# Kernel tuning notes

Measured on AMD Instinct MI355X. Metric: run time of the kernel, lower is better.

Reference implementation:

```python
import jax, jax.numpy as jnp
import numpy as np

N, B, H, L, FE = 32768, 256, 128, 4, 4
E = 262144


def setup_inputs() -> dict:
    key = jax.random.key(0)
    ks = jax.random.split(key, 16)
    def g(i, shape, scale=0.05):
        return jax.random.normal(ks[i], shape, dtype=jnp.float32) * scale
    return {
        "d": jax.random.uniform(ks[0], (E,), dtype=jnp.float32) * 5.0,
        "src": jax.random.randint(ks[1], (E,), 0, N),
        "dst": jax.random.randint(ks[2], (E,), 0, N),
        "seg": jnp.sort(jax.random.randint(ks[3], (N,), 0, B)),
        "node_emb": g(4, (H,), 1.0),
        "We": g(5, (2 * FE + 1, H)), "be": jnp.zeros((H,), jnp.float32),
        "msg_W1": g(6, (L, 3 * H, H)), "msg_b1": jnp.zeros((L, H), jnp.float32),
        "msg_W2": g(7, (L, H, H)), "msg_b2": jnp.zeros((L, H), jnp.float32),
        "soft_W": g(8, (L, H)), "soft_b": jnp.zeros((L,), jnp.float32),
        "upd_W1": g(9, (L, H, H)), "upd_b1": jnp.zeros((L, H), jnp.float32),
        "upd_W2": g(10, (L, H, H)), "upd_b2": jnp.zeros((L, H), jnp.float32),
        "out_W1": g(11, (H, H)), "out_b1": jnp.zeros((H,), jnp.float32),
        "out_W2": g(12, (H, H)), "out_b2": jnp.zeros((H,), jnp.float32),
    }


def reference(d, src, dst, seg, node_emb, We, be, msg_W1, msg_b1, msg_W2, msg_b2,
              soft_W, soft_b, upd_W1, upd_b1, upd_W2, upd_b2,
              out_W1, out_b1, out_W2, out_b2):
    silu = jax.nn.silu
    # fourier_encode_dist: [E] -> [E, 2*FE+1] = [sin(d/2^k), cos(d/2^k), d]
    scales = 2.0 ** jnp.arange(FE, dtype=d.dtype)
    x = d[:, None] / scales
    de = jnp.concatenate([jnp.sin(x), jnp.cos(x), d[:, None]], axis=-1)
    # edge_input MLP (1 layer, last_activation=SiLU) then extra F.silu in input_edge_func
    e = silu(silu(de @ We + be))                              # [E, H]
    # node_embedding broadcast to all nodes
    feat = jnp.broadcast_to(node_emb, (N, H))
    for l in range(L):
        mi = jnp.concatenate([feat[src], feat[dst], e], axis=-1)        # [E, 3H]
        m = silu(silu(mi @ msg_W1[l] + msg_b1[l]) @ msg_W2[l] + msg_b2[l])  # [E, H]
        e = e + m                                             # edge residual update
        w = jax.nn.sigmoid(m @ soft_W[l] + soft_b[l])[:, None]  # soft edge gate [E,1]
        msum = jax.ops.segment_sum(m * w, dst, num_segments=N)  # reduce to dst nodes
        upd_in = msum + feat
        feat = silu(upd_in @ upd_W1[l] + upd_b1[l]) @ upd_W2[l] + upd_b2[l] + feat
    # node-wise output network (2 layers, last activation None)
    feat = silu(feat @ out_W1 + out_b1) @ out_W2 + out_b2
    # multi-aggregator readout over graphs in batch
    s = jax.ops.segment_sum(feat, seg, num_segments=B)
    cnt = jax.ops.segment_sum(jnp.ones((N, 1), feat.dtype), seg, num_segments=B)
    mean = s / jnp.maximum(cnt, 1.0)
    mx = jax.ops.segment_max(feat, seg, num_segments=B)
    return jnp.concatenate([s, mean, mx], axis=-1)            # [B, 3H]
```

## Files before the change

kernel.cpp:

```cpp
#include <hip/hip_runtime.h>
#include <hip/hip_bf16.h>

#define NN 32768
#define NB 256
#define HD 128
#define NL 4
#define NE 262144

typedef short bf16x8 __attribute__((ext_vector_type(8)));
typedef float f32x4 __attribute__((ext_vector_type(4)));
typedef unsigned short u16;
typedef unsigned int u32;

__device__ __forceinline__ float bf2f(u16 u) {
  return __uint_as_float(((u32)u) << 16);
}
__device__ __forceinline__ u16 f2bf(float f) {
  u32 x = __float_as_uint(f);
  u32 r = x + 0x7FFFu + ((x >> 16) & 1u);
  return (u16)(r >> 16);
}
__device__ __forceinline__ u32 pk2(float a, float b) {
  __hip_bfloat162 h = __float22bfloat162_rn(make_float2(a, b));
  return *reinterpret_cast<u32*>(&h);
}
__device__ __forceinline__ float siluf(float x) {
  return x * __builtin_amdgcn_rcpf(1.0f + __expf(-x));
}
__device__ __forceinline__ float sigf(float x) {
  return __builtin_amdgcn_rcpf(1.0f + __expf(-x));
}
__device__ __forceinline__ u32 ordu(float f) {
  u32 b = __float_as_uint(f);
  return (b & 0x80000000u) ? ~b : (b | 0x80000000u);
}

__device__ __forceinline__ float ldinf(const void* p, size_t i, int mode) {
  return mode ? ((const float*)p)[i] : bf2f(((const u16*)p)[i]);
}
__device__ __forceinline__ u16 ldinb(const void* p, size_t i, int mode) {
  return mode ? f2bf(((const float*)p)[i]) : ((const u16*)p)[i];
}

__global__ void k_detect(const u16* __restrict__ Weraw, int* __restrict__ flag) {
  if (threadIdx.x == 0 && blockIdx.x == 0) {
    int cnt = 0;
    for (int i = 0; i < 256; i++) {
      u16 u = Weraw[2 * i];
      u32 e = (u >> 7) & 0xFFu;
      if (e >= 112u && e <= 126u) cnt++;
    }
    *flag = (cnt >= 128) ? 0 : 1;
  }
}


__global__ __launch_bounds__(256) void k_csr_deg(const int* __restrict__ dstp,
                                                 u32* __restrict__ deg) {
  const int i = blockIdx.x * 256 + threadIdx.x;
  atomicAdd(&deg[dstp[i]], 1u);
}

__global__ __launch_bounds__(1024) void k_csr_scan(const u32* __restrict__ deg,
                                                   int* __restrict__ rowptr,
                                                   int* __restrict__ cursor) {
  __shared__ int part[1024];
  const int t = threadIdx.x;
  int loc[32];
  int s = 0;
#pragma unroll
  for (int j = 0; j < 32; j++) { loc[j] = s; s += (int)deg[t * 32 + j]; }
  part[t] = s;
  __syncthreads();
  int inc = s;
  for (int off = 1; off < 1024; off <<= 1) {
    int tmp = (t >= off) ? part[t - off] : 0;
    __syncthreads();
    part[t] += tmp;
    __syncthreads();
  }
  const int base = part[t] - inc;
#pragma unroll
  for (int j = 0; j < 32; j++) {
    rowptr[t * 32 + j] = base + loc[j];
    cursor[t * 32 + j] = base + loc[j];
  }
  if (t == 1023) rowptr[NN] = part[1023];
}

__global__ __launch_bounds__(256) void k_csr_scatter(const int* __restrict__ dstp,
                                                     const int* __restrict__ srcp,
                                                     int* __restrict__ cursor,
                                                     int* __restrict__ eids,
                                                     int* __restrict__ src_s,
                                                     int* __restrict__ dst_s) {
  const int i = blockIdx.x * 256 + threadIdx.x;
  const int d = dstp[i];
  const int pos = atomicAdd(&cursor[d], 1);
  eids[pos] = i;
  src_s[pos] = srcp[i];
  dst_s[pos] = d;
}

#define PANEL 16384

template <int MT>
__device__ __forceinline__ void acc_zero(f32x4 (&acc)[MT][8]) {
#pragma unroll
  for (int mt = 0; mt < MT; mt++)
#pragma unroll
    for (int nt = 0; nt < 8; nt++) acc[mt][nt] = f32x4{0.f, 0.f, 0.f, 0.f};
}

template <int MT>
__device__ __forceinline__ void gemm_gp(const u16* __restrict__ A0,
                                        const size_t* rowoff,
                                        const u16* __restrict__ Bp,
                                        int l, int kg, f32x4 (&acc)[MT][8]) {
#pragma unroll
  for (int ks = 0; ks < 4; ks++) {
    bf16x8 a[MT];
#pragma unroll
    for (int mt = 0; mt < MT; mt++)
      a[mt] = *(const bf16x8*)&A0[rowoff[mt] + ks * 32 + kg * 8];
#pragma unroll
    for (int nt = 0; nt < 8; nt++) {
      bf16x8 b = *(const bf16x8*)&Bp[(size_t)((nt * 4 + ks) * 64 + l) * 8];
#pragma unroll
      for (int mt = 0; mt < MT; mt++)
        acc[mt][nt] = __builtin_amdgcn_mfma_f32_16x16x32_bf16(a[mt], b, acc[mt][nt], 0, 0, 0);
    }
  }
}

template <int MT>
__device__ __forceinline__ void wave_gemm_p(const short* lAw, const u16* __restrict__ Bp,
                                            int l, int c, int kg, f32x4 (&acc)[MT][8]) {
#pragma unroll
  for (int ks = 0; ks < 4; ks++) {
    bf16x8 a[MT];
#pragma unroll
    for (int mt = 0; mt < MT; mt++) {
      const int r = mt * 16 + c;
      const int k = ks * 32 + kg * 8;
      a[mt] = *(const bf16x8*)&lAw[r * HD + (k ^ ((r & 7) << 3))];
    }
#pragma unroll
    for (int nt = 0; nt < 8; nt++) {
      bf16x8 b = *(const bf16x8*)&Bp[(size_t)((nt * 4 + ks) * 64 + l) * 8];
#pragma unroll
      for (int mt = 0; mt < MT; mt++)
        acc[mt][nt] = __builtin_amdgcn_mfma_f32_16x16x32_bf16(a[mt], b, acc[mt][nt], 0, 0, 0);
    }
  }
}

template <int MT, bool SILU>
__device__ __forceinline__ void wave_pack(short* lAw, int c, int kg,
                                          f32x4 (&acc)[MT][8], const float* bias) {
#pragma unroll
  for (int mt = 0; mt < MT; mt++) {
#pragma unroll
    for (int rr = 0; rr < 4; rr++) {
      const int row = mt * 16 + kg * 4 + rr;
      u32 ou[4];
#pragma unroll
      for (int p = 0; p < 4; p++) {
        float x0 = acc[mt][2 * p][rr] + bias[2 * p];
        float x1 = acc[mt][2 * p + 1][rr] + bias[2 * p + 1];
        if (SILU) { x0 = siluf(x0); x1 = siluf(x1); }
        ou[p] = pk2(x0, x1);
      }
      ((int4*)(lAw + row * HD))[c ^ (row & 7)] =
          make_int4((int)ou[0], (int)ou[1], (int)ou[2], (int)ou[3]);
    }
  }
}

__global__ __launch_bounds__(256) void k_prep(
    const void* __restrict__ mW1, const void* __restrict__ mW2,
    const void* __restrict__ uW1, const void* __restrict__ uW2,
    const void* __restrict__ oW1, const void* __restrict__ oW2,
    const int* __restrict__ flagp,
    u16* __restrict__ Wt1, u16* __restrict__ Wt2p,
    u16* __restrict__ Wtu1, u16* __restrict__ Wtu2p,
    u16* __restrict__ Wto1, u16* __restrict__ Wto2p) {
  const int mode = *flagp;
  const int tid = blockIdx.x * blockDim.x + threadIdx.x;
  const int stride = gridDim.x * blockDim.x;
  for (int i = tid; i < NL * 3 * PANEL; i += stride) {
    const int l = i / (3 * PANEL), r = i % (3 * PANEL);
    const int chunk = r / PANEL, r2 = r % PANEL;
    const int nt = r2 / 2048, ks = (r2 % 2048) / 512;
    const int lane = (r2 % 512) / 8, j = r2 % 8;
    const int s = ks * 32 + (lane >> 4) * 8 + j;
    const int klog = ((s & 7) << 4) | (s >> 3);
    const int n = nt * 16 + (lane & 15);
    Wt1[i] = ldinb(mW1, ((size_t)l * 384 + chunk * 128 + klog) * HD + n, mode);
  }
  for (int i = tid; i < NL * PANEL; i += stride) {
    const int l = i / PANEL, r = i % PANEL;
    const int nt = r / 2048, ks = (r % 2048) / 512;
    const int lane = (r % 512) / 8, j = r % 8;
    const int s = ks * 32 + (lane >> 4) * 8 + j;
    const int klog = ((s & 7) << 4) | (s >> 3);
    const int n = nt * 16 + (lane & 15);
    Wt2p[i] = ldinb(mW2, ((size_t)l * HD + klog) * HD + n, mode);
    Wtu1[i] = ldinb(uW1, ((size_t)l * HD + klog) * HD + n, mode);
    Wtu2p[i] = ldinb(uW2, ((size_t)l * HD + klog) * HD + n, mode);
  }
  for (int i = tid; i < PANEL; i += stride) {
    const int nt = i / 2048, ks = (i % 2048) / 512;
    const int lane = (i % 512) / 8, j = i % 8;
    const int s = ks * 32 + (lane >> 4) * 8 + j;
    const int klog = ((s & 7) << 4) | (s >> 3);
    const int n = nt * 16 + (lane & 15);
    Wto1[i] = ldinb(oW1, (size_t)klog * HD + n, mode);
    Wto2p[i] = ldinb(oW2, (size_t)klog * HD + n, mode);
  }
}

__global__ __launch_bounds__(256) void k_featinit(const void* __restrict__ nemb,
                                                  const int* __restrict__ flagp,
                                                  u16* __restrict__ feat) {
  const int mode = *flagp;
  const int i = blockIdx.x * 256 + threadIdx.x;
  const int g = i & 15;
  u32 ou[4];
#pragma unroll
  for (int p = 0; p < 4; p++) {
    u16 a = ldinb(nemb, (2 * p) * 16 + g, mode);
    u16 b = ldinb(nemb, (2 * p + 1) * 16 + g, mode);
    ou[p] = (u32)a | ((u32)b << 16);
  }
  ((int4*)feat)[i] = make_int4((int)ou[0], (int)ou[1], (int)ou[2], (int)ou[3]);
}

__global__ __launch_bounds__(256) void k_encode(const void* __restrict__ d,
                                                const int* __restrict__ eids,
                                                const void* __restrict__ We,
                                                const void* __restrict__ be,
                                                const int* __restrict__ flagp,
                                                u16* __restrict__ e) {
  const int mode = *flagp;
  __shared__ float sW[9 * HD];
  __shared__ float sb[HD];
  for (int i = threadIdx.x; i < 9 * HD; i += 256) sW[i] = ldinf(We, i, mode);
  for (int i = threadIdx.x; i < HD; i += 256) sb[i] = ldinf(be, i, mode);
  __syncthreads();
  const int spos = blockIdx.x * 256 + threadIdx.x;
  const float dv = ldinf(d, eids[spos], mode);
  float de[9];
#pragma unroll
  for (int k = 0; k < 4; k++) {
    float x = dv * (1.0f / (float)(1 << k));
    de[k] = __sinf(x);
    de[4 + k] = __cosf(x);
  }
  de[8] = dv;
  u16* erow = e + (size_t)spos * HD;
#pragma unroll
  for (int g = 0; g < 16; g++) {
    u32 ou[4];
#pragma unroll
    for (int p = 0; p < 4; p++) {
      float vv[2];
#pragma unroll
      for (int t = 0; t < 2; t++) {
        const int h = (2 * p + t) * 16 + g;
        float a = sb[h];
#pragma unroll
        for (int k = 0; k < 9; k++) a += de[k] * sW[k * HD + h];
        vv[t] = siluf(siluf(a));
      }
      ou[p] = pk2(vv[0], vv[1]);
    }
    ((int4*)erow)[g] = make_int4((int)ou[0], (int)ou[1], (int)ou[2], (int)ou[3]);
  }
}

__global__ __launch_bounds__(64, 4) void k_edge(
    const u16* __restrict__ feat, u16* __restrict__ e,
    const int* __restrict__ src_s, const int* __restrict__ dst_s,
    const u16* __restrict__ Wt1, const u16* __restrict__ Wt2p,
    const void* __restrict__ b1g, const void* __restrict__ b2g,
    const void* __restrict__ softW, const void* __restrict__ softb,
    const int* __restrict__ flagp, float* __restrict__ msum, int layer) {
  __shared__ __align__(16) short lM[32 * HD];
  __shared__ float swg[32];
  __shared__ int sdst[32];
  const int mode = *flagp;
  const int l = threadIdx.x;
  const int c = l & 15, kg = l >> 4;
  const int blk = blockIdx.x * 32;

  if (l < 32) sdst[l] = dst_s[blk + l];

  size_t offS[2], offD[2], offE[2];
#pragma unroll
  for (int mt = 0; mt < 2; mt++) {
    const int eidx = blk + mt * 16 + c;
    offS[mt] = (size_t)src_s[eidx] * HD;
    offD[mt] = (size_t)dst_s[eidx] * HD;
    offE[mt] = (size_t)eidx * HD;
  }

  const u16* W1l = Wt1 + (size_t)layer * 3 * PANEL;
  const u16* W2l = Wt2p + (size_t)layer * PANEL;
  float bias1[8], bias2[8], swf[8];
#pragma unroll
  for (int nt = 0; nt < 8; nt++) {
    bias1[nt] = ldinf(b1g, layer * HD + nt * 16 + c, mode);
    bias2[nt] = ldinf(b2g, layer * HD + nt * 16 + c, mode);
    swf[nt] = ldinf(softW, (size_t)layer * HD + nt * 16 + c, mode);
  }
  const float sbv = ldinf(softb, layer, mode);

  f32x4 acc[2][8];
  acc_zero<2>(acc);
  gemm_gp<2>(feat, offS, W1l, l, kg, acc);
  gemm_gp<2>(feat, offD, W1l + PANEL, l, kg, acc);
  gemm_gp<2>(e, offE, W1l + 2 * PANEL, l, kg, acc);
  wave_pack<2, true>(lM, c, kg, acc, bias1);
  __syncthreads();

  acc_zero<2>(acc);
  wave_gemm_p<2>(lM, W2l, l, c, kg, acc);
  __syncthreads();

  float wred[2][4];
#pragma unroll
  for (int mt = 0; mt < 2; mt++) {
#pragma unroll
    for (int rr = 0; rr < 4; rr++) {
      const int row = mt * 16 + kg * 4 + rr;
      int4* erow4 = (int4*)(e + (size_t)(blk + row) * HD);
      const int4 eo = erow4[c];
      const u32 eu[4] = {(u32)eo.x, (u32)eo.y, (u32)eo.z, (u32)eo.w};
      float mv[8];
      float wp = 0.f;
#pragma unroll
      for (int nt = 0; nt < 8; nt++) {
        mv[nt] = siluf(acc[mt][nt][rr] + bias2[nt]);
        wp += mv[nt] * swf[nt];
      }
      u32 mo[4], ou[4];
#pragma unroll
      for (int p = 0; p < 4; p++) {
        mo[p] = pk2(mv[2 * p], mv[2 * p + 1]);
        ou[p] = pk2(bf2f((u16)(eu[p] & 0xffffu)) + mv[2 * p],
                    bf2f((u16)(eu[p] >> 16)) + mv[2 * p + 1]);
      }
      ((int4*)(lM + row * HD))[c ^ (row & 7)] =
          make_int4((int)mo[0], (int)mo[1], (int)mo[2], (int)mo[3]);
      erow4[c] = make_int4((int)ou[0], (int)ou[1], (int)ou[2], (int)ou[3]);
      wp += __shfl_xor(wp, 1);
      wp += __shfl_xor(wp, 2);
      wp += __shfl_xor(wp, 4);
      wp += __shfl_xor(wp, 8);
      wred[mt][rr] = wp;
    }
  }
#pragma unroll
  for (int mt = 0; mt < 2; mt++)
#pragma unroll
    for (int rr = 0; rr < 4; rr++)
      if (c == mt * 4 + rr) swg[mt * 16 + kg * 4 + rr] = sigf(wred[mt][rr] + sbv);
  __syncthreads();

  const int gM = ((l >> 3) << 3);
  const int em = l & 7;
  float a0 = 0.f, a1 = 0.f;
  int cur = sdst[0];
  for (int r = 0; r < 32; r++) {
    const int dn = sdst[r];
    if (dn != cur) {
      atomicAdd(&msum[(size_t)cur * HD + l], a0);
      atomicAdd(&msum[(size_t)cur * HD + l + 64], a1);
      a0 = 0.f; a1 = 0.f; cur = dn;
    }
    const int rx = (r & 7) << 3;
    const float wgr = swg[r];
    a0 += wgr * bf2f((u16)lM[r * HD + (gM ^ rx) + em]);
    a1 += wgr * bf2f((u16)lM[r * HD + (gM ^ rx) + 64 + em]);
  }
  atomicAdd(&msum[(size_t)cur * HD + l], a0);
  atomicAdd(&msum[(size_t)cur * HD + l + 64], a1);
}

__global__ __launch_bounds__(64, 4) void k_node(
    u16* __restrict__ feat, const float* __restrict__ msum,
    const u16* __restrict__ Wtu1, const u16* __restrict__ Wtu2p,
    const void* __restrict__ b1g, const void* __restrict__ b2g,
    const int* __restrict__ flagp, int layer) {
  __shared__ __align__(16) short lA[32 * HD];
  const int mode = *flagp;
  const int l = threadIdx.x;
  const int c = l & 15, kg = l >> 4;
  short* lAw = lA;
  const int blkn = blockIdx.x * 32;
  const u16* W1l = Wtu1 + (size_t)layer * PANEL;
  const u16* W2l = Wtu2p + (size_t)layer * PANEL;
  float bias1[8], bias2[8];
#pragma unroll
  for (int nt = 0; nt < 8; nt++) {
    bias1[nt] = ldinf(b1g, layer * HD + nt * 16 + c, mode);
    bias2[nt] = ldinf(b2g, layer * HD + nt * 16 + c, mode);
  }
#pragma unroll
  for (int rp = 0; rp < 8; rp++) {
    const int r = rp * 4 + (l >> 4);
    const int g = l & 15;
    const int4 fv = ((const int4*)(feat + (size_t)(blkn + r) * HD))[g];
    const u32 uu[4] = {(u32)fv.x, (u32)fv.y, (u32)fv.z, (u32)fv.w};
    const float4 ma = ((const float4*)(msum + (size_t)(blkn + r) * HD))[2 * g];
    const float4 mb = ((const float4*)(msum + (size_t)(blkn + r) * HD))[2 * g + 1];
    const float mm[8] = {ma.x, ma.y, ma.z, ma.w, mb.x, mb.y, mb.z, mb.w};
    u32 ou[4];
#pragma unroll
    for (int p = 0; p < 4; p++) {
      ou[p] = pk2(bf2f((u16)(uu[p] & 0xffffu)) + mm[2 * p],
                  bf2f((u16)(uu[p] >> 16)) + mm[2 * p + 1]);
    }
    ((int4*)(lAw + r * HD))[g ^ (r & 7)] =
        make_int4((int)ou[0], (int)ou[1], (int)ou[2], (int)ou[3]);
  }
  __syncthreads();
  f32x4 acc[2][8];
  acc_zero<2>(acc);
  wave_gemm_p<2>(lAw, W1l, l, c, kg, acc);
  __syncthreads();
  wave_pack<2, true>(lAw, c, kg, acc, bias1);
  __syncthreads();
  acc_zero<2>(acc);
  wave_gemm_p<2>(lAw, W2l, l, c, kg, acc);

#pragma unroll
  for (int mt = 0; mt < 2; mt++) {
#pragma unroll
    for (int rr = 0; rr < 4; rr++) {
      const int row = mt * 16 + kg * 4 + rr;
      int4* frow4 = (int4*)(feat + (size_t)(blkn + row) * HD);
      const int4 fo = frow4[c];
      const u32 fu[4] = {(u32)fo.x, (u32)fo.y, (u32)fo.z, (u32)fo.w};
      u32 ou[4];
#pragma unroll
      for (int p = 0; p < 4; p++) {
        const float x0 = acc[mt][2 * p][rr] + bias2[2 * p];
        const float x1 = acc[mt][2 * p + 1][rr] + bias2[2 * p + 1];
        ou[p] = pk2(bf2f((u16)(fu[p] & 0xffffu)) + x0,
                    bf2f((u16)(fu[p] >> 16)) + x1);
      }
      frow4[c] = make_int4((int)ou[0], (int)ou[1], (int)ou[2], (int)ou[3]);
    }
  }
}

__global__ __launch_bounds__(64, 4) void k_out(
    const u16* __restrict__ feat, const int* __restrict__ seg,
    const u16* __restrict__ Wto1, const u16* __restrict__ Wto2p,
    const void* __restrict__ ob1, const void* __restrict__ ob2,
    const int* __restrict__ flagp,
    float* __restrict__ sacc, u32* __restrict__ mxacc, float* __restrict__ cnt) {
  __shared__ __align__(16) short lA[32 * HD];
  __shared__ int sseg[32];
  const int mode = *flagp;
  const int l = threadIdx.x;
  const int c = l & 15, kg = l >> 4;
  short* lAw = lA;
  const int blkn = blockIdx.x * 32;
  float bias1[8], bias2[8];
#pragma unroll
  for (int nt = 0; nt < 8; nt++) {
    bias1[nt] = ldinf(ob1, nt * 16 + c, mode);
    bias2[nt] = ldinf(ob2, nt * 16 + c, mode);
  }
#pragma unroll
  for (int rp = 0; rp < 8; rp++) {
    const int r = rp * 4 + (l >> 4);
    const int g = l & 15;
    ((int4*)(lAw + r * HD))[g ^ (r & 7)] =
        ((const int4*)(feat + (size_t)(blkn + r) * HD))[g];
  }
  if (l < 32) sseg[l] = seg[blkn + l];
  __syncthreads();
  f32x4 acc[2][8];
  acc_zero<2>(acc);
  wave_gemm_p<2>(lAw, Wto1, l, c, kg, acc);
  __syncthreads();
  wave_pack<2, true>(lAw, c, kg, acc, bias1);
  __syncthreads();
  acc_zero<2>(acc);
  wave_gemm_p<2>(lAw, Wto2p, l, c, kg, acc);
  __syncthreads();
  wave_pack<2, false>(lAw, c, kg, acc, bias2);
  __syncthreads();

  const int gL = l >> 2;
  const int eoff = (l & 3) * 2;
  const bool uniform = (sseg[0] == sseg[31]);
  if (uniform) {
    const int g = sseg[0];
    float s1 = 0.f, s2 = 0.f, x1 = -3.402823e38f, x2 = -3.402823e38f;
#pragma unroll 4
    for (int r = 0; r < 32; r++) {
      const u32 mv = *(const u32*)&lAw[r * HD + ((gL ^ (r & 7)) << 3) + eoff];
      const float v1 = bf2f((u16)(mv & 0xffffu));
      const float v2 = bf2f((u16)(mv >> 16));
      s1 += v1; s2 += v2;
      x1 = fmaxf(x1, v1); x2 = fmaxf(x2, v2);
    }
    atomicAdd(&sacc[(size_t)g * HD + 2 * l], s1);
    atomicAdd(&sacc[(size_t)g * HD + 2 * l + 1], s2);
    atomicMax(&mxacc[(size_t)g * HD + 2 * l], ordu(x1));
    atomicMax(&mxacc[(size_t)g * HD + 2 * l + 1], ordu(x2));
    if (l == 0) atomicAdd(&cnt[g], 32.0f);
  } else {
    if (l < 32) atomicAdd(&cnt[sseg[l]], 1.0f);
#pragma unroll 4
    for (int r = 0; r < 32; r++) {
      const u32 mv = *(const u32*)&lAw[r * HD + ((gL ^ (r & 7)) << 3) + eoff];
      const float v1 = bf2f((u16)(mv & 0xffffu));
      const float v2 = bf2f((u16)(mv >> 16));
      const int g = sseg[r];
      atomicAdd(&sacc[(size_t)g * HD + 2 * l], v1);
      atomicAdd(&sacc[(size_t)g * HD + 2 * l + 1], v2);
      atomicMax(&mxacc[(size_t)g * HD + 2 * l], ordu(v1));
      atomicMax(&mxacc[(size_t)g * HD + 2 * l + 1], ordu(v2));
    }
  }
}

__global__ __launch_bounds__(256) void k_final(const float* __restrict__ sacc,
                                               const u32* __restrict__ mxacc,
                                               const float* __restrict__ cnt,
                                               const int* __restrict__ flagp,
                                               void* __restrict__ out) {
  const int mode = *flagp;
  const int i = blockIdx.x * 256 + threadIdx.x;
  const int b = i / 384, j = i % 384;
  float v;
  if (j < HD) {
    const int p = ((j & 15) << 3) | (j >> 4);
    v = sacc[b * HD + p];
  } else if (j < 2 * HD) {
    const int t = j - HD;
    const int p = ((t & 15) << 3) | (t >> 4);
    v = sacc[b * HD + p] / fmaxf(cnt[b], 1.0f);
  } else {
    const int t = j - 2 * HD;
    const int p = ((t & 15) << 3) | (t >> 4);
    u32 u = mxacc[b * HD + p];
    u32 bits = (u >> 31) ? (u ^ 0x80000000u) : ~u;
    v = __uint_as_float(bits);
  }
  if (mode) ((float*)out)[i] = v;
  else ((u16*)out)[i] = f2bf(v);
}

extern "C" void kernel_launch(void* const* d_in, const int* in_sizes, int n_in,
                              void* d_out, int out_size, void* d_ws, size_t ws_size,
                              hipStream_t stream) {
  const void* d_d = d_in[0];
  const int* src = (const int*)d_in[1];
  const int* dst = (const int*)d_in[2];
  const int* seg = (const int*)d_in[3];
  const void* nemb = d_in[4];
  const void* We = d_in[5];
  const void* be = d_in[6];
  const void* mW1 = d_in[7];
  const void* mb1 = d_in[8];
  const void* mW2 = d_in[9];
  const void* mb2 = d_in[10];
  const void* sW = d_in[11];
  const void* sb = d_in[12];
  const void* uW1 = d_in[13];
  const void* ub1 = d_in[14];
  const void* uW2 = d_in[15];
  const void* ub2 = d_in[16];
  const void* oW1 = d_in[17];
  const void* ob1 = d_in[18];
  const void* oW2 = d_in[19];
  const void* ob2 = d_in[20];

  char* ws = (char*)d_ws;
  const size_t OFF_E = 0;
  const size_t OFF_MSUM = OFF_E + (size_t)NE * HD * 2;
  const size_t OFF_FEAT = OFF_MSUM + (size_t)NN * HD * 4;
  const size_t OFF_SACC = OFF_FEAT + (size_t)NN * HD * 2;
  const size_t OFF_MX = OFF_SACC + (size_t)NB * HD * 4;
  const size_t OFF_CNT = OFF_MX + (size_t)NB * HD * 4;
  const size_t OFF_DEG = OFF_CNT + 1024;
  const size_t OFF_ROWPTR = OFF_DEG + (size_t)NN * 4;
  const size_t OFF_CURSOR = OFF_ROWPTR + (size_t)(NN + 2) * 4;
  const size_t OFF_EIDS = OFF_CURSOR + (size_t)NN * 4;
  const size_t OFF_SRCS = OFF_EIDS + (size_t)NE * 4;
  const size_t OFF_DSTS = OFF_SRCS + (size_t)NE * 4;
  const size_t OFF_WT1 = OFF_DSTS + (size_t)NE * 4;
  const size_t OFF_WT2P = OFF_WT1 + (size_t)NL * 3 * PANEL * 2;
  const size_t OFF_WTU1 = OFF_WT2P + (size_t)NL * PANEL * 2;
  const size_t OFF_WTU2P = OFF_WTU1 + (size_t)NL * PANEL * 2;
  const size_t OFF_WTO1 = OFF_WTU2P + (size_t)NL * PANEL * 2;
  const size_t OFF_WTO2P = OFF_WTO1 + (size_t)PANEL * 2;
  const size_t OFF_FLAG = OFF_WTO2P + (size_t)PANEL * 2;

  u16* e = (u16*)(ws + OFF_E);
  float* msum = (float*)(ws + OFF_MSUM);
  u16* feat = (u16*)(ws + OFF_FEAT);
  float* sacc = (float*)(ws + OFF_SACC);
  u32* mx = (u32*)(ws + OFF_MX);
  float* cnt = (float*)(ws + OFF_CNT);
  u32* deg = (u32*)(ws + OFF_DEG);
  int* rowptr = (int*)(ws + OFF_ROWPTR);
  int* cursor = (int*)(ws + OFF_CURSOR);
  int* eids = (int*)(ws + OFF_EIDS);
  int* src_s = (int*)(ws + OFF_SRCS);
  int* dst_s = (int*)(ws + OFF_DSTS);
  u16* Wt1 = (u16*)(ws + OFF_WT1);
  u16* Wt2p = (u16*)(ws + OFF_WT2P);
  u16* Wtu1 = (u16*)(ws + OFF_WTU1);
  u16* Wtu2p = (u16*)(ws + OFF_WTU2P);
  u16* Wto1 = (u16*)(ws + OFF_WTO1);
  u16* Wto2p = (u16*)(ws + OFF_WTO2P);
  int* flag = (int*)(ws + OFF_FLAG);

  hipMemsetAsync(ws + OFF_SACC, 0,
                 (size_t)NB * HD * 4 * 2 + 1024 + (size_t)NN * 4, stream);

  k_detect<<<1, 64, 0, stream>>>((const u16*)We, flag);
  k_prep<<<256, 256, 0, stream>>>(mW1, mW2, uW1, uW2, oW1, oW2, flag,
                                  Wt1, Wt2p, Wtu1, Wtu2p, Wto1, Wto2p);
  k_featinit<<<(NN * HD / 8) / 256, 256, 0, stream>>>(nemb, flag, feat);

  k_csr_deg<<<NE / 256, 256, 0, stream>>>(dst, deg);
  k_csr_scan<<<1, 1024, 0, stream>>>(deg, rowptr, cursor);
  k_csr_scatter<<<NE / 256, 256, 0, stream>>>(dst, src, cursor, eids, src_s, dst_s);

  k_encode<<<NE / 256, 256, 0, stream>>>(d_d, eids, We, be, flag, e);

  for (int l = 0; l < NL; l++) {
    hipMemsetAsync(msum, 0, (size_t)NN * HD * 4, stream);
    k_edge<<<NE / 32, 64, 0, stream>>>(feat, e, src_s, dst_s, Wt1, Wt2p,
                                       mb1, mb2, sW, sb, flag, msum, l);
    k_node<<<NN / 32, 64, 0, stream>>>(feat, msum, Wtu1, Wtu2p, ub1, ub2, flag, l);
  }
  k_out<<<NN / 32, 64, 0, stream>>>(feat, seg, Wto1, Wto2p, ob1, ob2, flag, sacc, mx, cnt);
  k_final<<<(NB * 384) / 256, 256, 0, stream>>>(sacc, mx, cnt, flag, d_out);
}
```

Baseline: 763.2 us.

## Halve edge tile to 16 rows and fold msum zeroing into node kernel

The edge kernel now handles 16 edges per block instead of 32. This halves the accumulator registers and shared memory, raises the launch bound to 5 blocks per SIMD, and defers the bias/soft-gate loads until after the GEMMs to cut register pressure. The per-layer memset of msum is replaced by having k_node zero each row after reading it, plus one initial memset. In exchange, every weight panel is reused over fewer rows, which adds weight traffic per edge, and the block-local run-merging before the atomics covers fewer rows, which may add atomics.

New measurement: 809.9 us. 1.06x slower.

```diff
diff --git a/kernel.cpp b/kernel.cpp
--- a/kernel.cpp
+++ b/kernel.cpp
@@ -279,100 +279,96 @@
   }
 }
 
-__global__ __launch_bounds__(64, 4) void k_edge(
+__global__ __launch_bounds__(64, 5) void k_edge(
     const u16* __restrict__ feat, u16* __restrict__ e,
     const int* __restrict__ src_s, const int* __restrict__ dst_s,
     const u16* __restrict__ Wt1, const u16* __restrict__ Wt2p,
     const void* __restrict__ b1g, const void* __restrict__ b2g,
     const void* __restrict__ softW, const void* __restrict__ softb,
     const int* __restrict__ flagp, float* __restrict__ msum, int layer) {
-  __shared__ __align__(16) short lM[32 * HD];
-  __shared__ float swg[32];
-  __shared__ int sdst[32];
+  __shared__ __align__(16) short lM[16 * HD];
+  __shared__ float swg[16];
+  __shared__ int sdst[16];
   const int mode = *flagp;
   const int l = threadIdx.x;
   const int c = l & 15, kg = l >> 4;
-  const int blk = blockIdx.x * 32;
-
-  if (l < 32) sdst[l] = dst_s[blk + l];
-
-  size_t offS[2], offD[2], offE[2];
-#pragma unroll
-  for (int mt = 0; mt < 2; mt++) {
-    const int eidx = blk + mt * 16 + c;
-    offS[mt] = (size_t)src_s[eidx] * HD;
-    offD[mt] = (size_t)dst_s[eidx] * HD;
-    offE[mt] = (size_t)eidx * HD;
-  }
+  const int blk = blockIdx.x * 16;
+
+  if (l < 16) sdst[l] = dst_s[blk + l];
+
+  size_t offS[1], offD[1], offE[1];
+  offS[0] = (size_t)src_s[blk + c] * HD;
+  offD[0] = (size_t)dst_s[blk + c] * HD;
+  offE[0] = (size_t)(blk + c) * HD;
 
   const u16* W1l = Wt1 + (size_t)layer * 3 * PANEL;
   const u16* W2l = Wt2p + (size_t)layer * PANEL;
-  float bias1[8], bias2[8], swf[8];
+
+  f32x4 acc[1][8];
+  acc_zero<1>(acc);
+  gemm_gp<1>(feat, offS, W1l, l, kg, acc);
+  gemm_gp<1>(feat, offD, W1l + PANEL, l, kg, acc);
+  gemm_gp<1>(e, offE, W1l + 2 * PANEL, l, kg, acc);
+
+  float bias1[8];
+#pragma unroll
+  for (int nt = 0; nt < 8; nt++)
+    bias1[nt] = ldinf(b1g, layer * HD + nt * 16 + c, mode);
+  wave_pack<1, true>(lM, c, kg, acc, bias1);
+  __syncthreads();
+
+  acc_zero<1>(acc);
+  wave_gemm_p<1>(lM, W2l, l, c, kg, acc);
+  __syncthreads();
+
+  float bias2[8], swf[8];
 #pragma unroll
   for (int nt = 0; nt < 8; nt++) {
-    bias1[nt] = ldinf(b1g, layer * HD + nt * 16 + c, mode);
     bias2[nt] = ldinf(b2g, layer * HD + nt * 16 + c, mode);
     swf[nt] = ldinf(softW, (size_t)layer * HD + nt * 16 + c, mode);
   }
   const float sbv = ldinf(softb, layer, mode);
 
-  f32x4 acc[2][8];
-  acc_zero<2>(acc);
-  gemm_gp<2>(feat, offS, W1l, l, kg, acc);
-  gemm_gp<2>(feat, offD, W1l + PANEL, l, kg, acc);
-  gemm_gp<2>(e, offE, W1l + 2 * PANEL, l, kg, acc);
-  wave_pack<2, true>(lM, c, kg, acc, bias1);
-  __syncthreads();
-
-  acc_zero<2>(acc);
-  wave_gemm_p<2>(lM, W2l, l, c, kg, acc);
-  __syncthreads();
-
-  float wred[2][4];
-#pragma unroll
-  for (int mt = 0; mt < 2; mt++) {
-#pragma unroll
-    for (int rr = 0; rr < 4; rr++) {
-      const int row = mt * 16 + kg * 4 + rr;
-      int4* erow4 = (int4*)(e + (size_t)(blk + row) * HD);
-      const int4 eo = erow4[c];
-      const u32 eu[4] = {(u32)eo.x, (u32)eo.y, (u32)eo.z, (u32)eo.w};
-      float mv[8];
-      float wp = 0.f;
-#pragma unroll
-      for (int nt = 0; nt < 8; nt++) {
-        mv[nt] = siluf(acc[mt][nt][rr] + bias2[nt]);
-        wp += mv[nt] * swf[nt];
-      }
-      u32 mo[4], ou[4];
-#pragma unroll
-      for (int p = 0; p < 4; p++) {
-        mo[p] = pk2(mv[2 * p], mv[2 * p + 1]);
-        ou[p] = pk2(bf2f((u16)(eu[p] & 0xffffu)) + mv[2 * p],
-                    bf2f((u16)(eu[p] >> 16)) + mv[2 * p + 1]);
-      }
-      ((int4*)(lM + row * HD))[c ^ (row & 7)] =
-          make_int4((int)mo[0], (int)mo[1], (int)mo[2], (int)mo[3]);
-      erow4[c] = make_int4((int)ou[0], (int)ou[1], (int)ou[2], (int)ou[3]);
-      wp += __shfl_xor(wp, 1);
-      wp += __shfl_xor(wp, 2);
-      wp += __shfl_xor(wp, 4);
-      wp += __shfl_xor(wp, 8);
-      wred[mt][rr] = wp;
-    }
-  }
-#pragma unroll
-  for (int mt = 0; mt < 2; mt++)
-#pragma unroll
-    for (int rr = 0; rr < 4; rr++)
-      if (c == mt * 4 + rr) swg[mt * 16 + kg * 4 + rr] = sigf(wred[mt][rr] + sbv);
+  float wred[4];
+#pragma unroll
+  for (int rr = 0; rr < 4; rr++) {
+    const int row = kg * 4 + rr;
+    int4* erow4 = (int4*)(e + (size_t)(blk + row) * HD);
+    const int4 eo = erow4[c];
+    const u32 eu[4] = {(u32)eo.x, (u32)eo.y, (u32)eo.z, (u32)eo.w};
+    float mv[8];
+    float wp = 0.f;
+#pragma unroll
+    for (int nt = 0; nt < 8; nt++) {
+      mv[nt] = siluf(acc[0][nt][rr] + bias2[nt]);
+      wp += mv[nt] * swf[nt];
+    }
+    u32 mo[4], ou[4];
+#pragma unroll
+    for (int p = 0; p < 4; p++) {
+      mo[p] = pk2(mv[2 * p], mv[2 * p + 1]);
+      ou[p] = pk2(bf2f((u16)(eu[p] & 0xffffu)) + mv[2 * p],
+                  bf2f((u16)(eu[p] >> 16)) + mv[2 * p + 1]);
+    }
+    ((int4*)(lM + row * HD))[c ^ (row & 7)] =
+        make_int4((int)mo[0], (int)mo[1], (int)mo[2], (int)mo[3]);
+    erow4[c] = make_int4((int)ou[0], (int)ou[1], (int)ou[2], (int)ou[3]);
+    wp += __shfl_xor(wp, 1);
+    wp += __shfl_xor(wp, 2);
+    wp += __shfl_xor(wp, 4);
+    wp += __shfl_xor(wp, 8);
+    wred[rr] = wp;
+  }
+#pragma unroll
+  for (int rr = 0; rr < 4; rr++)
+    if (c == rr) swg[kg * 4 + rr] = sigf(wred[rr] + sbv);
   __syncthreads();
 
   const int gM = ((l >> 3) << 3);
   const int em = l & 7;
   float a0 = 0.f, a1 = 0.f;
   int cur = sdst[0];
-  for (int r = 0; r < 32; r++) {
+  for (int r = 0; r < 16; r++) {
     const int dn = sdst[r];
     if (dn != cur) {
       atomicAdd(&msum[(size_t)cur * HD + l], a0);
@@ -389,7 +385,7 @@
 }
 
 __global__ __launch_bounds__(64, 4) void k_node(
-    u16* __restrict__ feat, const float* __restrict__ msum,
+    u16* __restrict__ feat, float* __restrict__ msum,
     const u16* __restrict__ Wtu1, const u16* __restrict__ Wtu2p,
     const void* __restrict__ b1g, const void* __restrict__ b2g,
     const int* __restrict__ flagp, int layer) {
@@ -407,14 +403,18 @@
     bias1[nt] = ldinf(b1g, layer * HD + nt * 16 + c, mode);
     bias2[nt] = ldinf(b2g, layer * HD + nt * 16 + c, mode);
   }
+  const float4 z4 = make_float4(0.f, 0.f, 0.f, 0.f);
 #pragma unroll
   for (int rp = 0; rp < 8; rp++) {
     const int r = rp * 4 + (l >> 4);
     const int g = l & 15;
     const int4 fv = ((const int4*)(feat + (size_t)(blkn + r) * HD))[g];
     const u32 uu[4] = {(u32)fv.x, (u32)fv.y, (u32)fv.z, (u32)fv.w};
-    const float4 ma = ((const float4*)(msum + (size_t)(blkn + r) * HD))[2 * g];
-    const float4 mb = ((const float4*)(msum + (size_t)(blkn + r) * HD))[2 * g + 1];
+    float4* mrow4 = (float4*)(msum + (size_t)(blkn + r) * HD);
+    const float4 ma = mrow4[2 * g];
+    const float4 mb = mrow4[2 * g + 1];
+    mrow4[2 * g] = z4;
+    mrow4[2 * g + 1] = z4;
     const float mm[8] = {ma.x, ma.y, ma.z, ma.w, mb.x, mb.y, mb.z, mb.w};
     u32 ou[4];
 #pragma unroll
@@ -626,6 +626,7 @@
 
   hipMemsetAsync(ws + OFF_SACC, 0,
                  (size_t)NB * HD * 4 * 2 + 1024 + (size_t)NN * 4, stream);
+  hipMemsetAsync(msum, 0, (size_t)NN * HD * 4, stream);
 
   k_detect<<<1, 64, 0, stream>>>((const u16*)We, flag);
   k_prep<<<256, 256, 0, stream>>>(mW1, mW2, uW1, uW2, oW1, oW2, flag,
@@ -639,8 +640,7 @@
   k_encode<<<NE / 256, 256, 0, stream>>>(d_d, eids, We, be, flag, e);
 
   for (int l = 0; l < NL; l++) {
-    hipMemsetAsync(msum, 0, (size_t)NN * HD * 4, stream);
-    k_edge<<<NE / 32, 64, 0, stream>>>(feat, e, src_s, dst_s, Wt1, Wt2p,
+    k_edge<<<NE / 16, 64, 0, stream>>>(feat, e, src_s, dst_s, Wt1, Wt2p,
                                        mb1, mb2, sW, sb, flag, msum, l);
     k_node<<<NN / 32, 64, 0, stream>>>(feat, msum, Wtu1, Wtu2p, ub1, ub2, flag, l);
   }
```
